# Kernel tuning notes

Measured on AMD Instinct MI355X. Metric: run time of the kernel, lower is better.

## Reference

```python
import jax, jax.numpy as jnp
import numpy as np

N_NODES = 100000
N_EDGES = 1600000
F_IN = 128
HID = 64
N_CLASSES = 1
N_GRAPHS = 1024


def gcn_conv(x, src, dst, deg_inv_sqrt, W, b):
    # PyG GCNConv: out = D^{-1/2}(A+I)D^{-1/2} X W + b
    xw = x @ W  # [N, H]
    norm = deg_inv_sqrt[src] * deg_inv_sqrt[dst]  # [E]
    msg = xw[src] * norm[:, None]  # gather + scale
    agg = jax.ops.segment_sum(msg, dst, num_segments=N_NODES)
    # self-loop contribution: norm_ii = deg_inv_sqrt[i]^2
    agg = agg + xw * (deg_inv_sqrt ** 2)[:, None]
    return agg + b


def setup_inputs() -> dict:
    key = jax.random.key(0)
    ks = jax.random.split(key, 12)
    x = jax.random.normal(ks[0], (N_NODES, F_IN), dtype=jnp.float32)
    edge_index = jax.random.randint(ks[1], (2, N_EDGES), 0, N_NODES, dtype=jnp.int64)
    batch = jnp.sort(jax.random.randint(ks[2], (N_NODES,), 0, N_GRAPHS, dtype=jnp.int64))
    def glorot(k, fan_in, fan_out):
        s = (6.0 / (fan_in + fan_out)) ** 0.5
        return jax.random.uniform(k, (fan_in, fan_out), dtype=jnp.float32, minval=-s, maxval=s)
    W1 = glorot(ks[3], F_IN, HID); b1 = jnp.zeros((HID,), jnp.float32)
    W2 = glorot(ks[4], HID, HID); b2 = jnp.zeros((HID,), jnp.float32)
    W3 = glorot(ks[5], HID, HID); b3 = jnp.zeros((HID,), jnp.float32)
    Wl = glorot(ks[6], HID, N_CLASSES); bl = jnp.zeros((N_CLASSES,), jnp.float32)
    return {"x": x, "edge_index": edge_index, "batch": batch,
            "W1": W1, "b1": b1, "W2": W2, "b2": b2, "W3": W3, "b3": b3,
            "Wl": Wl, "bl": bl}


def reference(x, edge_index, batch, W1, b1, W2, b2, W3, b3, Wl, bl):
    src, dst = edge_index[0], edge_index[1]
    # degree with self-loops: deg[i] = (# incoming edges at i) + 1
    deg = jax.ops.segment_sum(jnp.ones((N_EDGES,), x.dtype), dst, num_segments=N_NODES) + 1.0
    deg_inv_sqrt = jax.lax.rsqrt(deg)
    h = jax.nn.relu(gcn_conv(x, src, dst, deg_inv_sqrt, W1, b1))
    # dropout: identity in eval mode
    h = jax.nn.relu(gcn_conv(h, src, dst, deg_inv_sqrt, W2, b2))
    h = gcn_conv(h, src, dst, deg_inv_sqrt, W3, b3)
    # global_mean_pool over graph ids
    sums = jax.ops.segment_sum(h, batch, num_segments=N_GRAPHS)
    counts = jax.ops.segment_sum(jnp.ones((N_NODES,), h.dtype), batch, num_segments=N_GRAPHS)
    pooled = sums / jnp.maximum(counts, 1.0)[:, None]  # [G, HID]
    return pooled @ Wl + bl  # [G, num_classes]
```

## Files before the change

### kernel.cpp

```cpp
#include <hip/hip_runtime.h>
#include <hip/hip_bf16.h>

#define N_NODES 100000
#define N_EDGES 1600000
#define F_IN 128
#define HID 64
#define N_GRAPHS 1024

#define SH 9
#define NBU 196
#define NB 200
#define BCAP 9728
#define EPB 2048
#define NSLICE 2

typedef __attribute__((ext_vector_type(8))) short bf16x8;
typedef __attribute__((ext_vector_type(4))) float f32x4;
typedef __attribute__((ext_vector_type(4))) unsigned int u32x4;

__device__ __forceinline__ unsigned short f2bf(float f) {
    __hip_bfloat16 h = __float2bfloat16(f);
    return *reinterpret_cast<unsigned short*>(&h);
}
__device__ __forceinline__ float bf2f(unsigned int u) {
    return __uint_as_float(u << 16);
}

__device__ __forceinline__ float loadf(const void* p, size_t i, int f32) {
    if (f32) return ((const float*)p)[i];
    return __bfloat162float(((const __hip_bfloat16*)p)[i]);
}
__device__ __forceinline__ int loadi(const void* p, size_t i, int i64) {
    if (i64) return (int)((const long long*)p)[i];
    return ((const int*)p)[i];
}

__global__ void k_init(const unsigned int* __restrict__ xw_,
                       const unsigned int* __restrict__ ei_,
                       int* __restrict__ flags,
                       int* __restrict__ gcnt, int* __restrict__ bcnt) {
    __shared__ int cnt_f, cnt_i;
    int t = threadIdx.x;
    if (t == 0) { cnt_f = 0; cnt_i = 0; }
    __syncthreads();
    unsigned int w = xw_[t];
    unsigned int e = (w >> 7) & 0xFFu;
    if (e >= 100u && e <= 140u) atomicAdd(&cnt_f, 1);
    unsigned int iw = ei_[2 * t + 1];
    if (iw == 0u) atomicAdd(&cnt_i, 1);
    for (int i = t; i < N_GRAPHS; i += 256) gcnt[i] = 0;
    for (int i = t; i < NB; i += 256) bcnt[i] = 0;
    __syncthreads();
    if (t == 0) {
        flags[0] = (cnt_f < 180) ? 1 : 0;
        flags[1] = (cnt_i >= 128) ? 1 : 0;
    }
}

__global__ __launch_bounds__(256) void k_part(const void* __restrict__ ei,
                                              const void* __restrict__ batch,
                                              int* __restrict__ bcnt,
                                              int* __restrict__ gcnt,
                                              unsigned int* __restrict__ packed,
                                              const int* __restrict__ flags) {
    int I64 = flags[1];
    __shared__ int hist[NB];
    __shared__ int base[NB];
    __shared__ int ghist[N_GRAPHS];
    __shared__ unsigned int elds[EPB];
    __shared__ unsigned char ebkt[EPB];
    int t = threadIdx.x;
    if (t < NB) hist[t] = 0;
    for (int i = t; i < N_GRAPHS; i += 256) ghist[i] = 0;
    __syncthreads();
    if (t < 128) {
        int n = blockIdx.x * 128 + t;
        if (n < N_NODES) atomicAdd(&ghist[loadi(batch, n, I64)], 1);
    }
    int e0 = blockIdx.x * EPB;
#pragma unroll 4
    for (int it = 0; it < EPB / 256; ++it) {
        int idx = it * 256 + t;
        int e = e0 + idx;
        unsigned int pv = 0u;
        unsigned char bk = 0xFFu;
        if (e < N_EDGES) {
            int sN = loadi(ei, e, I64);
            int d = loadi(ei, (size_t)N_EDGES + e, I64);
            bk = (unsigned char)(d >> SH);
            pv = ((unsigned int)sN << SH) | (unsigned int)(d & 511);
            atomicAdd(&hist[d >> SH], 1);
        }
        elds[idx] = pv;
        ebkt[idx] = bk;
    }
    __syncthreads();
    if (t < NB) {
        base[t] = hist[t] ? atomicAdd(&bcnt[t], hist[t]) : 0;
        hist[t] = 0;
    }
    for (int i = t; i < N_GRAPHS; i += 256)
        if (ghist[i]) atomicAdd(&gcnt[i], ghist[i]);
    __syncthreads();
#pragma unroll 4
    for (int it = 0; it < EPB / 256; ++it) {
        int idx = it * 256 + t;
        unsigned char bk = ebkt[idx];
        if (bk != 0xFFu) {
            unsigned int pv = elds[idx];
            int r = atomicAdd(&hist[bk], 1);
            int pos = base[bk] + r;
            if (pos < BCAP)
                packed[(size_t)bk * BCAP + pos] = pv;
        }
    }
}

__global__ __launch_bounds__(512) void k_csr(const unsigned int* __restrict__ packed,
                                             const int* __restrict__ bcnt,
                                             float* __restrict__ dis,
                                             int2* __restrict__ rp2,
                                             int* __restrict__ csr,
                                             const int* __restrict__ gcnt,
                                             int* __restrict__ gptr) {
    __shared__ int hist[512];
    __shared__ int offs[512];
    __shared__ int elds[BCAP];
    int b = blockIdx.x;
    int t = threadIdx.x;
    if (b == NBU) {
        int a = gcnt[2 * t], bq = gcnt[2 * t + 1];
        int ps = a + bq;
        hist[t] = ps;
        __syncthreads();
        for (int off = 1; off < 512; off <<= 1) {
            int x = (t >= off) ? hist[t - off] : 0;
            __syncthreads();
            hist[t] += x;
            __syncthreads();
        }
        int excl = hist[t] - ps;
        gptr[2 * t] = excl;
        gptr[2 * t + 1] = excl + a;
        if (t == 511) gptr[1024] = hist[511];
        return;
    }
    int n = bcnt[b]; if (n > BCAP) n = BCAP;
    hist[t] = 0;
    __syncthreads();
    const unsigned int* pb = packed + (size_t)b * BCAP;
    for (int i = t; i < n; i += 512)
        atomicAdd(&hist[pb[i] & 511u], 1);
    __syncthreads();
    int c = hist[t];
    offs[t] = c;
    __syncthreads();
    for (int off = 1; off < 512; off <<= 1) {
        int x = (t >= off) ? offs[t - off] : 0;
        __syncthreads();
        offs[t] += x;
        __syncthreads();
    }
    int excl = offs[t] - c;
    int node = (b << SH) + t;
    int base = b * BCAP;
    if (node < N_NODES) {
        dis[node] = rsqrtf((float)c + 1.0f);
        rp2[node] = make_int2(base + excl, base + excl + c);
    }
    __syncthreads();
    offs[t] = excl;
    __syncthreads();
    for (int i = t; i < n; i += 512) {
        unsigned int p = pb[i];
        int pos = atomicAdd(&offs[p & 511u], 1);
        if (pos < BCAP) elds[pos] = (int)(p >> SH);
    }
    __syncthreads();
    for (int i = t; i < n; i += 512)
        csr[base + i] = elds[i];
}

template <int K>
__global__ __launch_bounds__(256) void k_gemm(const void* __restrict__ x,
                                              const void* __restrict__ W,
                                              const float* __restrict__ dis,
                                              unsigned short* __restrict__ out,
                                              const int* __restrict__ flags,
                                              int x_is_f32) {
    int Wf32 = flags[0];
    int xF32 = (x_is_f32 < 0) ? Wf32 : x_is_f32;
    __shared__ unsigned short Wt[64][K + 8];
    __shared__ unsigned short xs[32][K + 8];
    int t = threadIdx.x;
    int wave = t >> 6, lane = t & 63;
    int quad = lane >> 4, l16 = lane & 15;

    for (int id = t; id < 64 * K; id += 256) {
        int k = id >> 6, n = id & 63;
        Wt[n][k] = f2bf(loadf(W, id, Wf32));
    }
    __syncthreads();

    bf16x8 bfrag[K / 32];
#pragma unroll
    for (int c = 0; c < K / 32; ++c)
        bfrag[c] = *reinterpret_cast<bf16x8*>(&Wt[wave * 16 + l16][c * 32 + quad * 8]);

    const int ngroups = (N_NODES + 31) / 32;
    for (int g = blockIdx.x; g < ngroups; g += gridDim.x) {
        __syncthreads();
        int row0 = g * 32;
        for (int cid = t; cid < 4 * K; cid += 256) {
            int rr = cid / (K / 8), c8 = cid % (K / 8);
            int r = row0 + rr;
            u32x4 val = {0u, 0u, 0u, 0u};
            if (r < N_NODES) {
                size_t base = (size_t)r * K + c8 * 8;
                if (xF32) {
                    const u32x4* xp = (const u32x4*)x;
                    u32x4 q0 = xp[base / 4];
                    u32x4 q1 = xp[base / 4 + 1];
                    val.x = f2bf(__uint_as_float(q0.x)) | ((unsigned int)f2bf(__uint_as_float(q0.y)) << 16);
                    val.y = f2bf(__uint_as_float(q0.z)) | ((unsigned int)f2bf(__uint_as_float(q0.w)) << 16);
                    val.z = f2bf(__uint_as_float(q1.x)) | ((unsigned int)f2bf(__uint_as_float(q1.y)) << 16);
                    val.w = f2bf(__uint_as_float(q1.z)) | ((unsigned int)f2bf(__uint_as_float(q1.w)) << 16);
                } else {
                    val = ((const u32x4*)x)[base / 8];
                }
            }
            *reinterpret_cast<u32x4*>(&xs[rr][c8 * 8]) = val;
        }
        __syncthreads();

        f32x4 acc0 = {0.f, 0.f, 0.f, 0.f};
        f32x4 acc1 = {0.f, 0.f, 0.f, 0.f};
#pragma unroll
        for (int c = 0; c < K / 32; ++c) {
            bf16x8 a0 = *reinterpret_cast<bf16x8*>(&xs[l16][c * 32 + quad * 8]);
            bf16x8 a1 = *reinterpret_cast<bf16x8*>(&xs[16 + l16][c * 32 + quad * 8]);
            acc0 = __builtin_amdgcn_mfma_f32_16x16x32_bf16(a0, bfrag[c], acc0, 0, 0, 0);
            acc1 = __builtin_amdgcn_mfma_f32_16x16x32_bf16(a1, bfrag[c], acc1, 0, 0, 0);
        }
        int col = wave * 16 + l16;
        unsigned short* ow = out + (size_t)(col >> 5) * (N_NODES * 32);
        int f = col & 31;
#pragma unroll
        for (int reg = 0; reg < 4; ++reg) {
            int r0 = row0 + quad * 4 + reg;
            if (r0 < N_NODES) ow[(size_t)r0 * 32 + f] = f2bf(acc0[reg] * dis[r0]);
            int r1 = row0 + 16 + quad * 4 + reg;
            if (r1 < N_NODES) ow[(size_t)r1 * 32 + f] = f2bf(acc1[reg] * dis[r1]);
        }
    }
}

__global__ __launch_bounds__(256) void k_gather_sm(const int2* __restrict__ rp2,
                                                   const int* __restrict__ csr,
                                                   const float* __restrict__ dis,
                                                   const unsigned short* __restrict__ xws,
                                                   const void* __restrict__ bias,
                                                   unsigned short* __restrict__ out,
                                                   const int* __restrict__ flags) {
    int F32 = flags[0];
    int blk = blockIdx.x;
    int xcd = blk & 7;
    int s = xcd >> 2;
    int grp = ((blk >> 3) << 2) | (xcd & 3);
    int wave = threadIdx.x >> 6, lane = threadIdx.x & 63;
    int nodesub = lane >> 4;
    int eslot = (lane >> 2) & 3;
    int q = lane & 3;
    const u32x4* xs4 = (const u32x4*)(xws + (size_t)s * N_NODES * 32);
    u32x4* op = (u32x4*)out;
    float bb0 = loadf(bias, s * 32 + q * 8 + 0, F32);
    float bb1 = loadf(bias, s * 32 + q * 8 + 1, F32);
    float bb2 = loadf(bias, s * 32 + q * 8 + 2, F32);
    float bb3 = loadf(bias, s * 32 + q * 8 + 3, F32);
    float bb4 = loadf(bias, s * 32 + q * 8 + 4, F32);
    float bb5 = loadf(bias, s * 32 + q * 8 + 5, F32);
    float bb6 = loadf(bias, s * 32 + q * 8 + 6, F32);
    float bb7 = loadf(bias, s * 32 + q * 8 + 7, F32);
    int wbase = grp * 64 + wave * 16;

    for (int ni = 0; ni < 4; ++ni) {
        int node = wbase + ni * 4 + nodesub;
        int valid = node < N_NODES;
        int2 se = valid ? rp2[node] : make_int2(0, 0);
        int start = se.x, end = se.y;
        float a0 = 0.f, a1 = 0.f, a2 = 0.f, a3 = 0.f;
        float a4 = 0.f, a5 = 0.f, a6 = 0.f, a7 = 0.f;
        int j = start + eslot;
        if (j < end) {
            int src = csr[j];
            for (;;) {
                int jn = j + 4;
                int sn = (jn < end) ? csr[jn] : 0;
                u32x4 v = xs4[(size_t)src * 4 + q];
                a0 += bf2f(v.x & 0xFFFFu); a1 += bf2f(v.x >> 16);
                a2 += bf2f(v.y & 0xFFFFu); a3 += bf2f(v.y >> 16);
                a4 += bf2f(v.z & 0xFFFFu); a5 += bf2f(v.z >> 16);
                a6 += bf2f(v.w & 0xFFFFu); a7 += bf2f(v.w >> 16);
                if (jn >= end) break;
                j = jn; src = sn;
            }
        }
#pragma unroll
        for (int off = 4; off <= 8; off <<= 1) {
            a0 += __shfl_down(a0, off, 64); a1 += __shfl_down(a1, off, 64);
            a2 += __shfl_down(a2, off, 64); a3 += __shfl_down(a3, off, 64);
            a4 += __shfl_down(a4, off, 64); a5 += __shfl_down(a5, off, 64);
            a6 += __shfl_down(a6, off, 64); a7 += __shfl_down(a7, off, 64);
        }
        if (((lane & 12) == 0) && valid) {
            u32x4 sv = xs4[(size_t)node * 4 + q];
            float dn = dis[node];
            float v0 = fmaf(a0 + bf2f(sv.x & 0xFFFFu), dn, bb0);
            float v1 = fmaf(a1 + bf2f(sv.x >> 16),     dn, bb1);
            float v2 = fmaf(a2 + bf2f(sv.y & 0xFFFFu), dn, bb2);
            float v3 = fmaf(a3 + bf2f(sv.y >> 16),     dn, bb3);
            float v4 = fmaf(a4 + bf2f(sv.z & 0xFFFFu), dn, bb4);
            float v5 = fmaf(a5 + bf2f(sv.z >> 16),     dn, bb5);
            float v6 = fmaf(a6 + bf2f(sv.w & 0xFFFFu), dn, bb6);
            float v7 = fmaf(a7 + bf2f(sv.w >> 16),     dn, bb7);
            v0 = fmaxf(v0, 0.f) * dn; v1 = fmaxf(v1, 0.f) * dn;
            v2 = fmaxf(v2, 0.f) * dn; v3 = fmaxf(v3, 0.f) * dn;
            v4 = fmaxf(v4, 0.f) * dn; v5 = fmaxf(v5, 0.f) * dn;
            v6 = fmaxf(v6, 0.f) * dn; v7 = fmaxf(v7, 0.f) * dn;
            u32x4 o;
            o.x = (unsigned int)f2bf(v0) | ((unsigned int)f2bf(v1) << 16);
            o.y = (unsigned int)f2bf(v2) | ((unsigned int)f2bf(v3) << 16);
            o.z = (unsigned int)f2bf(v4) | ((unsigned int)f2bf(v5) << 16);
            o.w = (unsigned int)f2bf(v6) | ((unsigned int)f2bf(v7) << 16);
            op[(size_t)node * 8 + s * 4 + q] = o;
        }
    }
}

__global__ __launch_bounds__(256) void k_fgl(const int2* __restrict__ rp2,
                                             const int* __restrict__ csr,
                                             const float* __restrict__ dis,
                                             const unsigned short* __restrict__ hs_in,
                                             const void* __restrict__ W,
                                             const void* __restrict__ bias,
                                             unsigned short* __restrict__ out,
                                             int relu_scale,
                                             const int* __restrict__ flags) {
    int F32 = flags[0];
    __shared__ unsigned short Wt[64][72];
    __shared__ unsigned short xs[64][72];
    int t = threadIdx.x;
    int w = t >> 6, lane = t & 63;
    for (int id = t; id < 64 * 64; id += 256) {
        int k = id >> 6, n = id & 63;
        Wt[n][k] = f2bf(loadf(W, id, F32));
    }
    int node2 = lane >> 5;
    int oct = lane & 7;
    const u32x4* xr = (const u32x4*)hs_in;
    int wbase = blockIdx.x * 64 + w * 16;
#pragma unroll
    for (int p = 0; p < 8; ++p) {
        int node = wbase + p * 2 + node2;
        int valid = node < N_NODES;
        int2 se = valid ? rp2[node] : make_int2(0, 0);
        float a0 = 0.f, a1 = 0.f, a2 = 0.f, a3 = 0.f;
        float a4 = 0.f, a5 = 0.f, a6 = 0.f, a7 = 0.f;
        int j = se.x + ((lane >> 3) & 3);
        if (j < se.y) {
            int src = csr[j];
            for (;;) {
                int jn = j + 4;
                int sn = (jn < se.y) ? csr[jn] : 0;
                u32x4 v = xr[(size_t)src * 8 + oct];
                a0 += bf2f(v.x & 0xFFFFu); a1 += bf2f(v.x >> 16);
                a2 += bf2f(v.y & 0xFFFFu); a3 += bf2f(v.y >> 16);
                a4 += bf2f(v.z & 0xFFFFu); a5 += bf2f(v.z >> 16);
                a6 += bf2f(v.w & 0xFFFFu); a7 += bf2f(v.w >> 16);
                if (jn >= se.y) break;
                j = jn; src = sn;
            }
        }
#pragma unroll
        for (int off = 8; off <= 16; off <<= 1) {
            a0 += __shfl_down(a0, off, 64); a1 += __shfl_down(a1, off, 64);
            a2 += __shfl_down(a2, off, 64); a3 += __shfl_down(a3, off, 64);
            a4 += __shfl_down(a4, off, 64); a5 += __shfl_down(a5, off, 64);
            a6 += __shfl_down(a6, off, 64); a7 += __shfl_down(a7, off, 64);
        }
        if ((lane & 24) == 0) {
            u32x4 sv = {0u, 0u, 0u, 0u};
            float dn = 0.f;
            if (valid) { sv = xr[(size_t)node * 8 + oct]; dn = dis[node]; }
            float v0 = (a0 + bf2f(sv.x & 0xFFFFu)) * dn;
            float v1 = (a1 + bf2f(sv.x >> 16))     * dn;
            float v2 = (a2 + bf2f(sv.y & 0xFFFFu)) * dn;
            float v3 = (a3 + bf2f(sv.y >> 16))     * dn;
            float v4 = (a4 + bf2f(sv.z & 0xFFFFu)) * dn;
            float v5 = (a5 + bf2f(sv.z >> 16))     * dn;
            float v6 = (a6 + bf2f(sv.w & 0xFFFFu)) * dn;
            float v7 = (a7 + bf2f(sv.w >> 16))     * dn;
            u32x4 o;
            o.x = (unsigned int)f2bf(v0) | ((unsigned int)f2bf(v1) << 16);
            o.y = (unsigned int)f2bf(v2) | ((unsigned int)f2bf(v3) << 16);
            o.z = (unsigned int)f2bf(v4) | ((unsigned int)f2bf(v5) << 16);
            o.w = (unsigned int)f2bf(v6) | ((unsigned int)f2bf(v7) << 16);
            *reinterpret_cast<u32x4*>(&xs[w * 16 + p * 2 + node2][oct * 8]) = o;
        }
    }
    __syncthreads();
    int quad = lane >> 4, l16 = lane & 15;
    bf16x8 bfrag[2];
#pragma unroll
    for (int c = 0; c < 2; ++c)
        bfrag[c] = *reinterpret_cast<bf16x8*>(&Wt[w * 16 + l16][c * 32 + quad * 8]);
    f32x4 acc[4];
#pragma unroll
    for (int rg = 0; rg < 4; ++rg) acc[rg] = (f32x4){0.f, 0.f, 0.f, 0.f};
#pragma unroll
    for (int c = 0; c < 2; ++c) {
#pragma unroll
        for (int rg = 0; rg < 4; ++rg) {
            bf16x8 a = *reinterpret_cast<bf16x8*>(&xs[rg * 16 + l16][c * 32 + quad * 8]);
            acc[rg] = __builtin_amdgcn_mfma_f32_16x16x32_bf16(a, bfrag[c], acc[rg], 0, 0, 0);
        }
    }
    int col = w * 16 + l16;
    float bcol = loadf(bias, col, F32);
    int rbase = blockIdx.x * 64;
#pragma unroll
    for (int rg = 0; rg < 4; ++rg) {
#pragma unroll
        for (int reg = 0; reg < 4; ++reg) {
            int row = rbase + rg * 16 + quad * 4 + reg;
            if (row < N_NODES) {
                float v = acc[rg][reg] + bcol;
                if (relu_scale) v = fmaxf(v, 0.f) * dis[row];
                out[(size_t)row * 64 + col] = f2bf(v);
            }
        }
    }
}

__global__ __launch_bounds__(256) void k_pool_final(const int* __restrict__ gptr,
                             const unsigned short* __restrict__ h,
                             const void* __restrict__ Wl, const void* __restrict__ bl,
                             void* __restrict__ out, const int* __restrict__ flags) {
    int F32 = flags[0];
    __shared__ float part[4];
    int g = blockIdx.x;
    int w = threadIdx.x >> 6;
    int lane = threadIdx.x & 63;
    int nsub = lane >> 5;
    int up = lane & 31;
    int s0 = gptr[g], e0 = gptr[g + 1];
    const unsigned int* xr = (const unsigned int*)h;
    float a0 = 0.f, a1 = 0.f;
    for (int n = s0 + w * 2 + nsub; n < e0; n += 8) {
        unsigned int v = xr[(size_t)n * 32 + up];
        a0 += bf2f(v & 0xFFFFu);
        a1 += bf2f(v >> 16);
    }
    a0 += __shfl_down(a0, 32, 64);
    a1 += __shfl_down(a1, 32, 64);
    float v = 0.f;
    if (lane < 32) {
        float cnt = fmaxf((float)(e0 - s0), 1.0f);
        int f = up * 2;
        v = (a0 / cnt) * loadf(Wl, f, F32) + (a1 / cnt) * loadf(Wl, f + 1, F32);
    }
    v += __shfl_down(v, 16, 64);
    v += __shfl_down(v, 8, 64);
    v += __shfl_down(v, 4, 64);
    v += __shfl_down(v, 2, 64);
    v += __shfl_down(v, 1, 64);
    if (lane == 0) part[w] = v;
    __syncthreads();
    if (threadIdx.x == 0) {
        float r = part[0] + part[1] + part[2] + part[3] + loadf(bl, 0, F32);
        if (F32) ((float*)out)[g] = r;
        else     ((__hip_bfloat16*)out)[g] = __float2bfloat16(r);
    }
}

extern "C" void kernel_launch(void* const* d_in, const int* in_sizes, int n_in,
                              void* d_out, int out_size, void* d_ws, size_t ws_size,
                              hipStream_t stream) {
    const void* x     = d_in[0];
    const void* ei    = d_in[1];
    const void* batch = d_in[2];
    const void* W1 = d_in[3];
    const void* b1 = d_in[4];
    const void* W2 = d_in[5];
    const void* b2 = d_in[6];
    const void* W3 = d_in[7];
    const void* b3 = d_in[8];
    const void* Wl = d_in[9];
    const void* bl = d_in[10];

    float* dis   = (float*)d_ws;
    int2*  rp2   = (int2*)(dis + 100352);
    int*   csr   = (int*)(rp2 + 100352);
    int*   gcnt  = csr + NB * BCAP;
    int*   gptr  = gcnt + 1024;
    int*   bcnt  = gptr + 1056;
    int*   flags = bcnt + 256;
    unsigned int* packed = (unsigned int*)(flags + 16);
    unsigned short* bufA = (unsigned short*)(packed + (size_t)NB * BCAP);
    unsigned short* bufB = bufA + (size_t)N_NODES * 64;

    const int TB = 256;
    dim3 blk(TB);
    int gGA = 391 * 8;
    int gFG = (N_NODES + 63) / 64;

    k_init<<<1, blk, 0, stream>>>((const unsigned int*)x, (const unsigned int*)ei,
                                  flags, gcnt, bcnt);
    k_part<<<(N_EDGES + EPB - 1) / EPB, blk, 0, stream>>>(ei, batch, bcnt, gcnt, packed, flags);
    k_csr<<<NBU + 1, 512, 0, stream>>>(packed, bcnt, dis, rp2, csr, gcnt, gptr);

    k_gemm<F_IN><<<1024, blk, 0, stream>>>(x, W1, dis, bufA, flags, -1);
    k_gather_sm<<<gGA, blk, 0, stream>>>(rp2, csr, dis, bufA, b1, bufB, flags);
    k_fgl<<<gFG, blk, 0, stream>>>(rp2, csr, dis, bufB, W2, b2, bufA, 1, flags);
    k_fgl<<<gFG, blk, 0, stream>>>(rp2, csr, dis, bufA, W3, b3, bufB, 0, flags);

    k_pool_final<<<N_GRAPHS, blk, 0, stream>>>(gptr, bufB, Wl, bl, d_out, flags);
}
```

Baseline: 331.7 us.

## Fold third GCN layer into pooling via W3·Wl projection and pipeline gather loads

The final GCN layer and the mean-pool kernel are merged. Because pooling and the final linear layer are linear, W3 and Wl are pre-multiplied into a 64-vector, and the pool kernel aggregates neighbour features per graph directly. This removes one full gather-GEMM pass over all nodes and its intermediate write. The gather loops in the other kernels are also software-pipelined so the next feature row load is issued before the current accumulate. The pool kernel now does an edge gather per graph block with limited parallelism (1024 blocks over variable-size graphs), and it recomputes the W3·Wl product in every block.

```diff
diff --git a/kernel.cpp b/kernel.cpp
--- a/kernel.cpp
+++ b/kernel.cpp
@@ -287,23 +287,28 @@
         int node = wbase + ni * 4 + nodesub;
         int valid = node < N_NODES;
         int2 se = valid ? rp2[node] : make_int2(0, 0);
-        int start = se.x, end = se.y;
         float a0 = 0.f, a1 = 0.f, a2 = 0.f, a3 = 0.f;
         float a4 = 0.f, a5 = 0.f, a6 = 0.f, a7 = 0.f;
-        int j = start + eslot;
-        if (j < end) {
+        int j = se.x + eslot;
+        if (j < se.y) {
             int src = csr[j];
-            for (;;) {
-                int jn = j + 4;
-                int sn = (jn < end) ? csr[jn] : 0;
-                u32x4 v = xs4[(size_t)src * 4 + q];
-                a0 += bf2f(v.x & 0xFFFFu); a1 += bf2f(v.x >> 16);
-                a2 += bf2f(v.y & 0xFFFFu); a3 += bf2f(v.y >> 16);
-                a4 += bf2f(v.z & 0xFFFFu); a5 += bf2f(v.z >> 16);
-                a6 += bf2f(v.w & 0xFFFFu); a7 += bf2f(v.w >> 16);
-                if (jn >= end) break;
-                j = jn; src = sn;
+            u32x4 vc = xs4[(size_t)src * 4 + q];
+            int jn = j + 4;
+            int sn = (jn < se.y) ? csr[jn] : 0;
+            while (jn < se.y) {
+                u32x4 vn = xs4[(size_t)sn * 4 + q];
+                int jn2 = jn + 4;
+                int sn2 = (jn2 < se.y) ? csr[jn2] : 0;
+                a0 += bf2f(vc.x & 0xFFFFu); a1 += bf2f(vc.x >> 16);
+                a2 += bf2f(vc.y & 0xFFFFu); a3 += bf2f(vc.y >> 16);
+                a4 += bf2f(vc.z & 0xFFFFu); a5 += bf2f(vc.z >> 16);
+                a6 += bf2f(vc.w & 0xFFFFu); a7 += bf2f(vc.w >> 16);
+                vc = vn; sn = sn2; jn = jn2;
             }
+            a0 += bf2f(vc.x & 0xFFFFu); a1 += bf2f(vc.x >> 16);
+            a2 += bf2f(vc.y & 0xFFFFu); a3 += bf2f(vc.y >> 16);
+            a4 += bf2f(vc.z & 0xFFFFu); a5 += bf2f(vc.z >> 16);
+            a6 += bf2f(vc.w & 0xFFFFu); a7 += bf2f(vc.w >> 16);
         }
 #pragma unroll
         for (int off = 4; off <= 8; off <<= 1) {
@@ -369,17 +374,23 @@
         int j = se.x + ((lane >> 3) & 3);
         if (j < se.y) {
             int src = csr[j];
-            for (;;) {
-                int jn = j + 4;
-                int sn = (jn < se.y) ? csr[jn] : 0;
-                u32x4 v = xr[(size_t)src * 8 + oct];
-                a0 += bf2f(v.x & 0xFFFFu); a1 += bf2f(v.x >> 16);
-                a2 += bf2f(v.y & 0xFFFFu); a3 += bf2f(v.y >> 16);
-                a4 += bf2f(v.z & 0xFFFFu); a5 += bf2f(v.z >> 16);
-                a6 += bf2f(v.w & 0xFFFFu); a7 += bf2f(v.w >> 16);
-                if (jn >= se.y) break;
-                j = jn; src = sn;
+            u32x4 vc = xr[(size_t)src * 8 + oct];
+            int jn = j + 4;
+            int sn = (jn < se.y) ? csr[jn] : 0;
+            while (jn < se.y) {
+                u32x4 vn = xr[(size_t)sn * 8 + oct];
+                int jn2 = jn + 4;
+                int sn2 = (jn2 < se.y) ? csr[jn2] : 0;
+                a0 += bf2f(vc.x & 0xFFFFu); a1 += bf2f(vc.x >> 16);
+                a2 += bf2f(vc.y & 0xFFFFu); a3 += bf2f(vc.y >> 16);
+                a4 += bf2f(vc.z & 0xFFFFu); a5 += bf2f(vc.z >> 16);
+                a6 += bf2f(vc.w & 0xFFFFu); a7 += bf2f(vc.w >> 16);
+                vc = vn; sn = sn2; jn = jn2;
             }
+            a0 += bf2f(vc.x & 0xFFFFu); a1 += bf2f(vc.x >> 16);
+            a2 += bf2f(vc.y & 0xFFFFu); a3 += bf2f(vc.y >> 16);
+            a4 += bf2f(vc.z & 0xFFFFu); a5 += bf2f(vc.z >> 16);
+            a6 += bf2f(vc.w & 0xFFFFu); a7 += bf2f(vc.w >> 16);
         }
 #pragma unroll
         for (int off = 8; off <= 16; off <<= 1) {
@@ -442,42 +453,102 @@
     }
 }
 
-__global__ __launch_bounds__(256) void k_pool_final(const int* __restrict__ gptr,
-                             const unsigned short* __restrict__ h,
-                             const void* __restrict__ Wl, const void* __restrict__ bl,
-                             void* __restrict__ out, const int* __restrict__ flags) {
+__global__ __launch_bounds__(256) void k_pool3(const int* __restrict__ gptr,
+                                               const int2* __restrict__ rp2,
+                                               const int* __restrict__ csr,
+                                               const float* __restrict__ dis,
+                                               const unsigned short* __restrict__ hs,
+                                               const void* __restrict__ W3,
+                                               const void* __restrict__ b3,
+                                               const void* __restrict__ Wl,
+                                               const void* __restrict__ bl,
+                                               void* __restrict__ out,
+                                               const int* __restrict__ flags) {
     int F32 = flags[0];
+    __shared__ float w3l[64];
     __shared__ float part[4];
+    __shared__ float cterm;
+    int t = threadIdx.x;
+    if (t < 64) {
+        float acc = 0.f;
+        for (int k = 0; k < 64; ++k)
+            acc += loadf(W3, t * 64 + k, F32) * loadf(Wl, k, F32);
+        w3l[t] = acc;
+    }
+    if (t == 64) {
+        float acc = 0.f;
+        for (int k = 0; k < 64; ++k)
+            acc += loadf(b3, k, F32) * loadf(Wl, k, F32);
+        cterm = acc;
+    }
+    __syncthreads();
     int g = blockIdx.x;
-    int w = threadIdx.x >> 6;
-    int lane = threadIdx.x & 63;
-    int nsub = lane >> 5;
-    int up = lane & 31;
+    int w = t >> 6, lane = t & 63;
+    int eslot = lane >> 3, oct = lane & 7;
     int s0 = gptr[g], e0 = gptr[g + 1];
-    const unsigned int* xr = (const unsigned int*)h;
-    float a0 = 0.f, a1 = 0.f;
-    for (int n = s0 + w * 2 + nsub; n < e0; n += 8) {
-        unsigned int v = xr[(size_t)n * 32 + up];
-        a0 += bf2f(v & 0xFFFFu);
-        a1 += bf2f(v >> 16);
-    }
-    a0 += __shfl_down(a0, 32, 64);
-    a1 += __shfl_down(a1, 32, 64);
+    const u32x4* xr = (const u32x4*)hs;
+    float P0 = 0.f, P1 = 0.f, P2 = 0.f, P3 = 0.f;
+    float P4 = 0.f, P5 = 0.f, P6 = 0.f, P7 = 0.f;
+    for (int node = s0 + w; node < e0; node += 4) {
+        int2 se = rp2[node];
+        float t0 = 0.f, t1 = 0.f, t2 = 0.f, t3 = 0.f;
+        float t4 = 0.f, t5 = 0.f, t6 = 0.f, t7 = 0.f;
+        int j = se.x + eslot;
+        if (j < se.y) {
+            int src = csr[j];
+            u32x4 vc = xr[(size_t)src * 8 + oct];
+            int jn = j + 8;
+            int sn = (jn < se.y) ? csr[jn] : 0;
+            while (jn < se.y) {
+                u32x4 vn = xr[(size_t)sn * 8 + oct];
+                int jn2 = jn + 8;
+                int sn2 = (jn2 < se.y) ? csr[jn2] : 0;
+                t0 += bf2f(vc.x & 0xFFFFu); t1 += bf2f(vc.x >> 16);
+                t2 += bf2f(vc.y & 0xFFFFu); t3 += bf2f(vc.y >> 16);
+                t4 += bf2f(vc.z & 0xFFFFu); t5 += bf2f(vc.z >> 16);
+                t6 += bf2f(vc.w & 0xFFFFu); t7 += bf2f(vc.w >> 16);
+                vc = vn; sn = sn2; jn = jn2;
+            }
+            t0 += bf2f(vc.x & 0xFFFFu); t1 += bf2f(vc.x >> 16);
+            t2 += bf2f(vc.y & 0xFFFFu); t3 += bf2f(vc.y >> 16);
+            t4 += bf2f(vc.z & 0xFFFFu); t5 += bf2f(vc.z >> 16);
+            t6 += bf2f(vc.w & 0xFFFFu); t7 += bf2f(vc.w >> 16);
+        }
+        if (eslot == 0) {
+            u32x4 sv = xr[(size_t)node * 8 + oct];
+            t0 += bf2f(sv.x & 0xFFFFu); t1 += bf2f(sv.x >> 16);
+            t2 += bf2f(sv.y & 0xFFFFu); t3 += bf2f(sv.y >> 16);
+            t4 += bf2f(sv.z & 0xFFFFu); t5 += bf2f(sv.z >> 16);
+            t6 += bf2f(sv.w & 0xFFFFu); t7 += bf2f(sv.w >> 16);
+        }
+        float dn = dis[node];
+        P0 = fmaf(t0, dn, P0); P1 = fmaf(t1, dn, P1);
+        P2 = fmaf(t2, dn, P2); P3 = fmaf(t3, dn, P3);
+        P4 = fmaf(t4, dn, P4); P5 = fmaf(t5, dn, P5);
+        P6 = fmaf(t6, dn, P6); P7 = fmaf(t7, dn, P7);
+    }
+#pragma unroll
+    for (int off = 8; off <= 32; off <<= 1) {
+        P0 += __shfl_down(P0, off, 64); P1 += __shfl_down(P1, off, 64);
+        P2 += __shfl_down(P2, off, 64); P3 += __shfl_down(P3, off, 64);
+        P4 += __shfl_down(P4, off, 64); P5 += __shfl_down(P5, off, 64);
+        P6 += __shfl_down(P6, off, 64); P7 += __shfl_down(P7, off, 64);
+    }
     float v = 0.f;
-    if (lane < 32) {
-        float cnt = fmaxf((float)(e0 - s0), 1.0f);
-        int f = up * 2;
-        v = (a0 / cnt) * loadf(Wl, f, F32) + (a1 / cnt) * loadf(Wl, f + 1, F32);
-    }
-    v += __shfl_down(v, 16, 64);
-    v += __shfl_down(v, 8, 64);
+    if (eslot == 0) {
+        int f = oct * 8;
+        v = P0 * w3l[f] + P1 * w3l[f + 1] + P2 * w3l[f + 2] + P3 * w3l[f + 3]
+          + P4 * w3l[f + 4] + P5 * w3l[f + 5] + P6 * w3l[f + 6] + P7 * w3l[f + 7];
+    }
     v += __shfl_down(v, 4, 64);
     v += __shfl_down(v, 2, 64);
     v += __shfl_down(v, 1, 64);
     if (lane == 0) part[w] = v;
     __syncthreads();
-    if (threadIdx.x == 0) {
-        float r = part[0] + part[1] + part[2] + part[3] + loadf(bl, 0, F32);
+    if (t == 0) {
+        float cnt = fmaxf((float)(e0 - s0), 1.0f);
+        float r = (part[0] + part[1] + part[2] + part[3]) / cnt
+                + ((e0 > s0) ? cterm : 0.f) + loadf(bl, 0, F32);
         if (F32) ((float*)out)[g] = r;
         else     ((__hip_bfloat16*)out)[g] = __float2bfloat16(r);
     }
@@ -522,7 +593,6 @@
     k_gemm<F_IN><<<1024, blk, 0, stream>>>(x, W1, dis, bufA, flags, -1);
     k_gather_sm<<<gGA, blk, 0, stream>>>(rp2, csr, dis, bufA, b1, bufB, flags);
     k_fgl<<<gFG, blk, 0, stream>>>(rp2, csr, dis, bufB, W2, b2, bufA, 1, flags);
-    k_fgl<<<gFG, blk, 0, stream>>>(rp2, csr, dis, bufA, W3, b3, bufB, 0, flags);
-
-    k_pool_final<<<N_GRAPHS, blk, 0, stream>>>(gptr, bufB, Wl, bl, d_out, flags);
-}
+    k_pool3<<<N_GRAPHS, blk, 0, stream>>>(gptr, rp2, csr, dis, bufA,
+                                          W3, b3, Wl, bl, d_out, flags);
+}
```

Measured after the change: 342.3 us. +3.2%, slower.
